# Performance work log

Measured on AMD Instinct MI355X. Metric: run time of the kernel, lower is better.

The kernel has to match this reference:

```python
import jax, jax.numpy as jnp
import numpy as np

B, H, W = 64, 512, 512          # batch, image height/width
BH, BW = 8, 8                   # block_size
K = 256                         # n_blocks (codebook size)
L = BH * BW                     # block_len = 64
HT, WT = H // BH, W // BW       # tiles per axis
T = HT * WT                     # tiles_per_img = 4096
BETA = 35.0


def _unfold(img):
    # img: (B, 1, H, W) -> patches (B, T, L), matching torch.nn.Unfold
    # with kernel=stride=(BH,BW): tiles row-major, patch flattened (kh, kw).
    x = img.reshape(B, 1, HT, BH, WT, BW)
    x = x.transpose(0, 2, 4, 1, 3, 5)          # (B, HT, WT, 1, BH, BW)
    return x.reshape(B, T, L)


def _fold(patches):
    # patches: (B, T, L) -> img (B, 1, H, W); exact inverse of _unfold
    # (non-overlapping, so Fold is pure reassembly, no accumulation).
    x = patches.reshape(B, HT, WT, 1, BH, BW)
    x = x.transpose(0, 3, 1, 4, 2, 5)          # (B, 1, HT, BH, WT, BW)
    return x.reshape(B, 1, H, W)


def setup_inputs() -> dict:
    key = jax.random.key(0)
    k1, k2 = jax.random.split(key)
    target_img = jax.random.uniform(k1, (B, 1, H, W), dtype=jnp.float32)
    # Learned codebook parameter (Haar-ish init in the original; values
    # don't change the math being tested).
    blocks = jax.random.uniform(k2, (K, BH, BW), dtype=jnp.float32)
    return {"target_img": target_img, "blocks": blocks}


def reference(target_img, blocks):
    patches = _unfold(target_img).reshape(B * T, L)   # (N, L), N = B*T
    codes = blocks.reshape(K, L)                      # (K, L)

    # Squared distances ||a - b||^2 via the expanded form to avoid
    # materializing the (N, K, L) difference tensor.
    a2 = jnp.sum(patches * patches, axis=-1, keepdims=True)   # (N, 1)
    b2 = jnp.sum(codes * codes, axis=-1)                      # (K,)
    ab = patches @ codes.T                                    # (N, K)
    sqerr = a2 - 2.0 * ab + b2                                # (N, K)

    block_weights = jax.nn.softmax(-BETA * sqerr, axis=-1)    # (N, K)
    uf_reconstructed = block_weights @ codes                  # (N, L)

    reconstructed = _fold(uf_reconstructed.reshape(B, T, L))  # (B,1,H,W)
    choice_penalty = jnp.mean(
        jnp.minimum(block_weights, 1.0 - block_weights)) * K
    return reconstructed, choice_penalty
```

## Files before the change

### kernel.cpp

```cpp
#include <hip/hip_runtime.h>


typedef short short8 __attribute__((ext_vector_type(8)));
typedef float floatx4 __attribute__((ext_vector_type(4)));

namespace {
constexpr float BETA_C = 35.0f;
constexpr float TAU    = 1e-6f;
constexpr float INV_N  = 1.0f / 262144.0f;
constexpr size_t IMG_ELEMS = (size_t)64 * 512 * 512;
constexpr int WB0 = 0;
constexpr int WB1 = 4096;
constexpr int WR  = 0;
constexpr int WS  = 4352;
constexpr int NWORDS = 8192;
}

__device__ __forceinline__ unsigned short f2bf(float x) {
  unsigned u = __float_as_uint(x);
  return (unsigned short)((u + 0x7FFFu + ((u >> 16) & 1u)) >> 16);
}
__device__ __forceinline__ float bf2f(unsigned short h) {
  return __uint_as_float((unsigned)h << 16);
}
__device__ __forceinline__ unsigned pack2(unsigned short lo, unsigned short hi) {
  return (unsigned)lo | ((unsigned)hi << 16);
}
__device__ __forceinline__ void cvt8t(float4 a, float4 b, short8& h, short8& l) {
  float f[8] = {a.x, a.y, a.z, a.w, b.x, b.y, b.z, b.w};
#pragma unroll
  for (int i = 0; i < 8; ++i) {
    unsigned short hh = f2bf(f[i]);
    h[i] = (short)hh;
    float lf = f[i] - bf2f(hh);
    l[i] = (short)(__float_as_uint(lf) >> 16);
  }
}
__device__ __forceinline__ void cp16(const uint4* g, unsigned* l) {
  __builtin_amdgcn_global_load_lds(
      (const __attribute__((address_space(1))) void*)g,
      (__attribute__((address_space(3))) void*)l, 16, 0, 0);
}

__global__ void pack_codes(const float* __restrict__ blk,
                           unsigned* __restrict__ wsBh,
                           unsigned* __restrict__ wsBl,
                           float* __restrict__ wsB2) {
  const int c = threadIdx.x;
  const float* src = blk + c * 64;
  float b2 = 0.f;
#pragma unroll
  for (int g = 0; g < 8; ++g) {
    int slot = c * 8 + (g ^ (c & 7));
#pragma unroll
    for (int t = 0; t < 4; ++t) {
      float v0 = src[g * 8 + 2 * t], v1 = src[g * 8 + 2 * t + 1];
      b2 += v0 * v0 + v1 * v1;
      unsigned short h0 = f2bf(v0), h1 = f2bf(v1);
      unsigned short l0 = f2bf(v0 - bf2f(h0)), l1 = f2bf(v1 - bf2f(h1));
      wsBh[slot * 4 + t] = pack2(h0, h1);
      wsBl[slot * 4 + t] = pack2(l0, l1);
    }
  }
  wsB2[c] = -BETA_C * b2;
}

__global__ __launch_bounds__(256, 5) void recon_kernel(
    const float* __restrict__ img, const float* __restrict__ blk,
    const unsigned* __restrict__ wsBh, const unsigned* __restrict__ wsBl,
    const float* __restrict__ wsB2, float* __restrict__ out,
    float* __restrict__ penAcc) {
  __shared__ unsigned sMem[NWORDS];
  float* sMemF = reinterpret_cast<float*>(sMem);

  const int tid = threadIdx.x;
  const int lane = tid & 63;
  const int wave = tid >> 6;
  const int b = blockIdx.x >> 6;
  const int ht = blockIdx.x & 63;
  const int c15 = lane & 15;
  const int q = lane >> 4;

  const float* imgBase = img + (size_t)b * (512 * 512) + (size_t)(ht * 8) * 512;
  const float* aptr = imgBase + q * 512 + (wave * 16 + c15) * 8;
  float4 v00 = *reinterpret_cast<const float4*>(aptr);
  float4 v01 = *reinterpret_cast<const float4*>(aptr + 4);
  float4 v10 = *reinterpret_cast<const float4*>(aptr + 2048);
  float4 v11 = *reinterpret_cast<const float4*>(aptr + 2048 + 4);

  const uint4* srcH = reinterpret_cast<const uint4*>(wsBh);
  const uint4* srcL = reinterpret_cast<const uint4*>(wsBl);
#pragma unroll
  for (int i = 0; i < 4; ++i) {
    cp16(srcH + i * 256 + tid, &sMem[WB0 + (i * 4 + wave) * 256]);
    cp16(srcL + i * 256 + tid, &sMem[WB1 + (i * 4 + wave) * 256]);
  }

  short8 ah[2], al[2];
  cvt8t(v00, v01, ah[0], al[0]);
  cvt8t(v10, v11, ah[1], al[1]);

  asm volatile("s_waitcnt vmcnt(0)" ::: "memory");
  __syncthreads();

  const int kx = c15 & 7;
  const unsigned* pb0 = &sMem[(8 * c15 + (q ^ kx)) * 4];
  const unsigned* pb1 = &sMem[(8 * c15 + ((q ^ 4) ^ kx)) * 4];

  float m[4], sm[4];
  float rr[16] = {0.f, 0.f, 0.f, 0.f, 0.f, 0.f, 0.f, 0.f,
                  0.f, 0.f, 0.f, 0.f, 0.f, 0.f, 0.f, 0.f};

#pragma unroll
  for (int h = 0; h < 2; ++h) {
    floatx4 acc[8];
#pragma unroll
    for (int n = 0; n < 8; ++n) acc[n] = (floatx4){0.f, 0.f, 0.f, 0.f};
#pragma unroll
    for (int n = 0; n < 8; ++n) {
      short8 b0h = *reinterpret_cast<const short8*>(pb0 + 512 * n);
      short8 b1h = *reinterpret_cast<const short8*>(pb1 + 512 * n);
      short8 b0l = *reinterpret_cast<const short8*>(pb0 + WB1 + 512 * n);
      short8 b1l = *reinterpret_cast<const short8*>(pb1 + WB1 + 512 * n);
      acc[n] = __builtin_amdgcn_mfma_f32_16x16x32_bf16(ah[0], b0h, acc[n], 0, 0, 0);
      acc[n] = __builtin_amdgcn_mfma_f32_16x16x32_bf16(al[0], b0h, acc[n], 0, 0, 0);
      acc[n] = __builtin_amdgcn_mfma_f32_16x16x32_bf16(ah[1], b1h, acc[n], 0, 0, 0);
      acc[n] = __builtin_amdgcn_mfma_f32_16x16x32_bf16(al[1], b1h, acc[n], 0, 0, 0);
      acc[n] = __builtin_amdgcn_mfma_f32_16x16x32_bf16(ah[0], b0l, acc[n], 0, 0, 0);
      acc[n] = __builtin_amdgcn_mfma_f32_16x16x32_bf16(ah[1], b1l, acc[n], 0, 0, 0);
    }
    if (h == 0) {
      __syncthreads();
#pragma unroll
      for (int i = 0; i < 4; ++i) {
        cp16(srcH + 1024 + i * 256 + tid, &sMem[WB0 + (i * 4 + wave) * 256]);
        cp16(srcL + 1024 + i * 256 + tid, &sMem[WB1 + (i * 4 + wave) * 256]);
      }
    }

#pragma unroll
    for (int n = 0; n < 8; ++n) {
      float b2s = wsB2[128 * h + 16 * n + c15];
#pragma unroll
      for (int r = 0; r < 4; ++r)
        acc[n][r] = fmaf(2.0f * BETA_C, acc[n][r], b2s);
    }
    float M[4];
#pragma unroll
    for (int r = 0; r < 4; ++r) {
      float mm = acc[0][r];
#pragma unroll
      for (int n = 1; n < 8; ++n) mm = fmaxf(mm, acc[n][r]);
#pragma unroll
      for (int off = 1; off <= 8; off <<= 1) mm = fmaxf(mm, __shfl_xor(mm, off, 64));
      M[r] = mm;
    }
    if (h == 0) {
#pragma unroll
      for (int r = 0; r < 4; ++r) { m[r] = M[r]; sm[r] = 0.f; }
    } else {
      float scl[4];
#pragma unroll
      for (int r = 0; r < 4; ++r) {
        float mn = fmaxf(m[r], M[r]);
        scl[r] = __expf(m[r] - mn);
        m[r] = mn;
        sm[r] *= scl[r];
      }
#pragma unroll
      for (int qq = 0; qq < 4; ++qq)
#pragma unroll
        for (int r = 0; r < 4; ++r) {
          float sq = __shfl(scl[r], qq * 16 + c15, 64);
          rr[4 * qq + r] *= sq;
        }
    }
#pragma unroll
    for (int n = 0; n < 8; ++n)
#pragma unroll
      for (int r = 0; r < 4; ++r) {
        float e = __expf(acc[n][r] - m[r]);
        acc[n][r] = e;
        sm[r] += e;
      }
#pragma unroll
    for (int n = 0; n < 8; ++n) {
      float em = fmaxf(fmaxf(acc[n][0], acc[n][1]), fmaxf(acc[n][2], acc[n][3]));
      unsigned long long msk = __ballot(em > TAU);
      while (msk) {
        int L = __builtin_ctzll(msk);
        msk &= msk - 1;
        float w0 = __uint_as_float(__builtin_amdgcn_readlane(__float_as_uint(acc[n][0]), L));
        float w1 = __uint_as_float(__builtin_amdgcn_readlane(__float_as_uint(acc[n][1]), L));
        float w2 = __uint_as_float(__builtin_amdgcn_readlane(__float_as_uint(acc[n][2]), L));
        float w3 = __uint_as_float(__builtin_amdgcn_readlane(__float_as_uint(acc[n][3]), L));
        float bv = blk[(size_t)(128 * h + 16 * n + (L & 15)) * 64 + lane];
        switch (L >> 4) {
          case 0: rr[0] += w0 * bv;  rr[1] += w1 * bv;  rr[2] += w2 * bv;  rr[3] += w3 * bv;  break;
          case 1: rr[4] += w0 * bv;  rr[5] += w1 * bv;  rr[6] += w2 * bv;  rr[7] += w3 * bv;  break;
          case 2: rr[8] += w0 * bv;  rr[9] += w1 * bv;  rr[10] += w2 * bv; rr[11] += w3 * bv; break;
          default: rr[12] += w0 * bv; rr[13] += w1 * bv; rr[14] += w2 * bv; rr[15] += w3 * bv; break;
        }
      }
    }
    if (h == 0) {
      asm volatile("s_waitcnt vmcnt(0)" ::: "memory");
      __syncthreads();
    }
  }

  float invS[4];
#pragma unroll
  for (int r = 0; r < 4; ++r) {
#pragma unroll
    for (int off = 1; off <= 8; off <<= 1) sm[r] += __shfl_xor(sm[r], off, 64);
    invS[r] = 1.0f / sm[r];
  }
  float pen = 0.f;
  if (c15 == 0) {
#pragma unroll
    for (int r = 0; r < 4; ++r)
      pen += (invS[r] > 0.5f) ? (2.0f - 2.0f * invS[r]) : 1.0f;
  }
  pen += __shfl_xor(pen, 16, 64);
  pen += __shfl_xor(pen, 32, 64);
  if (lane == 0) atomicAdd(penAcc, pen * INV_N);

  __syncthreads();

  if (c15 == 0) {
#pragma unroll
    for (int r = 0; r < 4; ++r)
      sMemF[WS + wave * 16 + 4 * q + r] = invS[r];
  }
#pragma unroll
  for (int pl = 0; pl < 16; ++pl)
    sMemF[WR + (wave * 16 + pl) * 68 + lane] = rr[pl];
  float* outBase = out + (size_t)b * (512 * 512) + (size_t)(ht * 8) * 512 +
                   wave * 128;
#pragma unroll
  for (int i = 0; i < 4; ++i) {
    int f = i * 64 + lane;
    int row = f >> 5;
    int cc = f & 31;
    int wtl = cc >> 1, hw = cc & 1;
    float4 v = *reinterpret_cast<const float4*>(
        &sMemF[WR + (wave * 16 + wtl) * 68 + row * 8 + hw * 4]);
    float is = sMemF[WS + wave * 16 + wtl];
    v.x *= is; v.y *= is; v.z *= is; v.w *= is;
    *reinterpret_cast<float4*>(outBase + row * 512 + cc * 4) = v;
  }
}

extern "C" void kernel_launch(void* const* d_in, const int* in_sizes, int n_in,
                              void* d_out, int out_size, void* d_ws, size_t ws_size,
                              hipStream_t stream) {
  const float* img = (const float*)d_in[0];
  const float* blk = (const float*)d_in[1];
  float* out = (float*)d_out;
  float* penSlot = out + IMG_ELEMS;

  unsigned* wsBh = (unsigned*)d_ws;
  unsigned* wsBl = wsBh + 8192;
  float* wsB2 = (float*)(wsBl + 8192);

  pack_codes<<<dim3(1), dim3(256), 0, stream>>>(blk, wsBh, wsBl, wsB2);
  hipMemsetAsync(penSlot, 0, sizeof(float), stream);
  recon_kernel<<<dim3(4096), dim3(256), 0, stream>>>(img, blk, wsBh, wsBl,
                                                     wsB2, out, penSlot);
}
```

Before: 347.2 us.

## Parallelize codebook packing, skip redundant rescale, lower occupancy bound

The codebook packing kernel now runs on 8 blocks, with one thread per 8-element group instead of one thread per code. It uses vectorized loads and stores and reduces the squared norm with shuffles. In the online softmax, the shuffle-based rescale of the accumulated reconstruction is skipped when no lane's running max changed. The recon kernel's launch bound drops from 5 to 4 waves per SIMD, giving the compiler more registers at the cost of occupancy.

```diff
diff --git a/kernel.cpp b/kernel.cpp
--- a/kernel.cpp
+++ b/kernel.cpp
@@ -46,26 +46,35 @@
                            unsigned* __restrict__ wsBh,
                            unsigned* __restrict__ wsBl,
                            float* __restrict__ wsB2) {
-  const int c = threadIdx.x;
-  const float* src = blk + c * 64;
+  const int gid = blockIdx.x * 256 + threadIdx.x;
+  const int c = gid >> 3, g = gid & 7;
+  const float* src = blk + c * 64 + g * 8;
+  float4 a = *reinterpret_cast<const float4*>(src);
+  float4 b = *reinterpret_cast<const float4*>(src + 4);
+  float f[8] = {a.x, a.y, a.z, a.w, b.x, b.y, b.z, b.w};
+  uint4 ph, pl;
+  unsigned* phw = reinterpret_cast<unsigned*>(&ph);
+  unsigned* plw = reinterpret_cast<unsigned*>(&pl);
   float b2 = 0.f;
 #pragma unroll
-  for (int g = 0; g < 8; ++g) {
-    int slot = c * 8 + (g ^ (c & 7));
-#pragma unroll
-    for (int t = 0; t < 4; ++t) {
-      float v0 = src[g * 8 + 2 * t], v1 = src[g * 8 + 2 * t + 1];
-      b2 += v0 * v0 + v1 * v1;
-      unsigned short h0 = f2bf(v0), h1 = f2bf(v1);
-      unsigned short l0 = f2bf(v0 - bf2f(h0)), l1 = f2bf(v1 - bf2f(h1));
-      wsBh[slot * 4 + t] = pack2(h0, h1);
-      wsBl[slot * 4 + t] = pack2(l0, l1);
-    }
-  }
-  wsB2[c] = -BETA_C * b2;
-}
-
-__global__ __launch_bounds__(256, 5) void recon_kernel(
+  for (int t = 0; t < 4; ++t) {
+    float v0 = f[2 * t], v1 = f[2 * t + 1];
+    b2 += v0 * v0 + v1 * v1;
+    unsigned short h0 = f2bf(v0), h1 = f2bf(v1);
+    unsigned short l0 = f2bf(v0 - bf2f(h0)), l1 = f2bf(v1 - bf2f(h1));
+    phw[t] = pack2(h0, h1);
+    plw[t] = pack2(l0, l1);
+  }
+  const int slot = c * 8 + (g ^ (c & 7));
+  reinterpret_cast<uint4*>(wsBh)[slot] = ph;
+  reinterpret_cast<uint4*>(wsBl)[slot] = pl;
+  b2 += __shfl_xor(b2, 1, 64);
+  b2 += __shfl_xor(b2, 2, 64);
+  b2 += __shfl_xor(b2, 4, 64);
+  if (g == 0) wsB2[c] = -BETA_C * b2;
+}
+
+__global__ __launch_bounds__(256, 4) void recon_kernel(
     const float* __restrict__ img, const float* __restrict__ blk,
     const unsigned* __restrict__ wsBh, const unsigned* __restrict__ wsBl,
     const float* __restrict__ wsB2, float* __restrict__ out,
@@ -167,13 +176,16 @@
         m[r] = mn;
         sm[r] *= scl[r];
       }
-#pragma unroll
-      for (int qq = 0; qq < 4; ++qq)
-#pragma unroll
-        for (int r = 0; r < 4; ++r) {
-          float sq = __shfl(scl[r], qq * 16 + c15, 64);
-          rr[4 * qq + r] *= sq;
-        }
+      bool moved = (scl[0] < 1.f) | (scl[1] < 1.f) | (scl[2] < 1.f) | (scl[3] < 1.f);
+      if (__any(moved)) {
+#pragma unroll
+        for (int qq = 0; qq < 4; ++qq)
+#pragma unroll
+          for (int r = 0; r < 4; ++r) {
+            float sq = __shfl(scl[r], qq * 16 + c15, 64);
+            rr[4 * qq + r] *= sq;
+          }
+      }
     }
 #pragma unroll
     for (int n = 0; n < 8; ++n)
@@ -264,7 +276,7 @@
   unsigned* wsBl = wsBh + 8192;
   float* wsB2 = (float*)(wsBl + 8192);
 
-  pack_codes<<<dim3(1), dim3(256), 0, stream>>>(blk, wsBh, wsBl, wsB2);
+  pack_codes<<<dim3(8), dim3(256), 0, stream>>>(blk, wsBh, wsBl, wsB2);
   hipMemsetAsync(penSlot, 0, sizeof(float), stream);
   recon_kernel<<<dim3(4096), dim3(256), 0, stream>>>(img, blk, wsBh, wsBl,
                                                      wsB2, out, penSlot);
```

Result: faster. 326.4 us (-6.0%).
